# Performance work log

Measured on AMD Instinct MI355X. Metric: run time of the kernel, lower is better.

Reference implementation:

```python
import jax, jax.numpy as jnp
import numpy as np

N, D = 50000, 1000
FH1, FH2 = 256, 128
GH1, GH2, H = 64, 30, 3
NC = 10
E = 800000
BN_EPS = 1e-5


def setup_inputs() -> dict:
    key = jax.random.key(0)
    ks = iter(jax.random.split(key, 48))
    nk = lambda: next(ks)
    r = lambda *s: jax.random.normal(nk(), s, jnp.float32) * 0.05
    g = lambda n: 1.0 + jax.random.normal(nk(), (n,), jnp.float32) * 0.01
    return dict(
        x=jax.random.normal(nk(), (N, D), jnp.float32),
        edge_index=jax.random.randint(nk(), (2, E), 0, N, dtype=jnp.int32),
        enc_w1=r(D, FH1), enc_b1=r(FH1), enc_g1=g(FH1), enc_bt1=r(FH1),
        enc_w2=r(FH1, FH2), enc_b2=r(FH2), enc_g2=g(FH2), enc_bt2=r(FH2),
        gat1_w=r(FH2, H * GH1), gat1_asrc=r(H, GH1), gat1_adst=r(H, GH1), gat1_b=r(H * GH1),
        gat2_w=r(H * GH1, GH2), gat2_asrc=r(1, GH2), gat2_adst=r(1, GH2), gat2_b=r(GH2),
        gat3_w=r(H * GH1, GH2), gat3_asrc=r(1, GH2), gat3_adst=r(1, GH2), gat3_b=r(GH2),
        dec_w1=r(GH2, FH2), dec_b1=r(FH2), dec_g1=g(FH2), dec_bt1=r(FH2),
        dec_w2=r(FH2, FH1), dec_b2=r(FH1), dec_g2=g(FH1), dec_bt2=r(FH1),
        dec_w3=r(FH1, D), dec_b3=r(D),
        clu_w1=r(GH2, FH2), clu_b1=r(FH2), clu_g1=g(FH2), clu_bt1=r(FH2),
        clu_w2=r(FH2, NC), clu_b2=r(NC),
    )


def _bn_elu(h, w, b, gm, bt):
    # Linear -> BatchNorm1d (batch stats) -> ELU; dropout is identity at eval
    h = h @ w + b
    m = h.mean(0)
    v = h.var(0)
    return jax.nn.elu(gm * (h - m) * jax.lax.rsqrt(v + BN_EPS) + bt)


def _gat(h, src, dst, n, w, a_src, a_dst, b, heads, oc, concat):
    # PyG GATConv: per-head linear, edge-wise LeakyReLU(0.2) scores,
    # softmax over incoming edges of each dst node, weighted scatter-sum.
    hh = (h @ w).reshape(n, heads, oc)            # [N,H,C]
    s_src = jnp.sum(hh * a_src, -1)               # [N,H]
    s_dst = jnp.sum(hh * a_dst, -1)               # [N,H]
    e = jax.nn.leaky_relu(s_src[src] + s_dst[dst], negative_slope=0.2)  # [E,H]
    m = jax.ops.segment_max(e, dst, num_segments=n)
    p = jnp.exp(e - m[dst])
    denom = jax.ops.segment_sum(p, dst, num_segments=n)
    alpha = p / denom[dst]                        # [E,H]
    msg = hh[src] * alpha[..., None]              # [E,H,C]
    out = jax.ops.segment_sum(msg, dst, num_segments=n)
    out = out.reshape(n, heads * oc) if concat else out.mean(1)
    return out + b


def reference(x, edge_index,
              enc_w1, enc_b1, enc_g1, enc_bt1, enc_w2, enc_b2, enc_g2, enc_bt2,
              gat1_w, gat1_asrc, gat1_adst, gat1_b,
              gat2_w, gat2_asrc, gat2_adst, gat2_b,
              gat3_w, gat3_asrc, gat3_adst, gat3_b,
              dec_w1, dec_b1, dec_g1, dec_bt1, dec_w2, dec_b2, dec_g2, dec_bt2, dec_w3, dec_b3,
              clu_w1, clu_b1, clu_g1, clu_bt1, clu_w2, clu_b2):
    n = x.shape[0]
    loops = jnp.arange(n, dtype=edge_index.dtype)  # GATConv add_self_loops=True
    src = jnp.concatenate([edge_index[0], loops])
    dst = jnp.concatenate([edge_index[1], loops])

    h = _bn_elu(x, enc_w1, enc_b1, enc_g1, enc_bt1)
    h = _bn_elu(h, enc_w2, enc_b2, enc_g2, enc_bt2)
    h = jax.nn.relu(_gat(h, src, dst, n, gat1_w, gat1_asrc, gat1_adst, gat1_b, H, GH1, True))
    mu = _gat(h, src, dst, n, gat2_w, gat2_asrc, gat2_adst, gat2_b, 1, GH2, False)
    logvar = _gat(h, src, dst, n, gat3_w, gat3_asrc, gat3_adst, gat3_b, 1, GH2, False)
    z = mu  # eval-mode reparameterize returns mu

    d = _bn_elu(z, dec_w1, dec_b1, dec_g1, dec_bt1)
    d = _bn_elu(d, dec_w2, dec_b2, dec_g2, dec_bt2)
    x_rec = d @ dec_w3 + dec_b3

    c = _bn_elu(z, clu_w1, clu_b1, clu_g1, clu_bt1)
    pred = jax.nn.softmax(c @ clu_w2 + clu_b2, axis=1)
    return (pred, x_rec, z, mu, logvar)
```

## Files before the change

### kernel.cpp

```cpp
#include <hip/hip_runtime.h>
#include <hip/hip_bf16.h>

typedef short short8 __attribute__((ext_vector_type(8)));
typedef short short4v __attribute__((ext_vector_type(4)));
typedef float f32x4 __attribute__((ext_vector_type(4)));

static __device__ __forceinline__ short f2bf(float f){
  __hip_bfloat16 h = __float2bfloat16(f);
  return __builtin_bit_cast(short, h);
}
static __device__ __forceinline__ float b2f(short s){
  unsigned int u = ((unsigned int)(unsigned short)s) << 16;
  return __builtin_bit_cast(float, u);
}
static __device__ __forceinline__ float lrelu(float x){ return x > 0.f ? x : 0.2f*x; }
static __device__ __forceinline__ float eluf(float x){ return x > 0.f ? x : (__expf(x)-1.f); }
static __device__ __forceinline__ int imin(int a,int b){ return a<b?a:b; }

typedef const __attribute__((address_space(1))) void as1_void;
typedef __attribute__((address_space(3))) void as3_void;
static __device__ __forceinline__ void gload16(const void* g, void* l){
  __builtin_amdgcn_global_load_lds((as1_void*)g, (as3_void*)l, 16, 0, 0);
}
template<int NN> __device__ __forceinline__ void wait_vm(){
  if constexpr (NN==0) asm volatile("s_waitcnt vmcnt(0)" ::: "memory");
  else if constexpr (NN==3) asm volatile("s_waitcnt vmcnt(3)" ::: "memory");
  else if constexpr (NN==4) asm volatile("s_waitcnt vmcnt(4)" ::: "memory");
  else if constexpr (NN==6) asm volatile("s_waitcnt vmcnt(6)" ::: "memory");
  else if constexpr (NN==8) asm volatile("s_waitcnt vmcnt(8)" ::: "memory");
  else if constexpr (NN==12) asm volatile("s_waitcnt vmcnt(12)" ::: "memory");
  else asm volatile("s_waitcnt vmcnt(0)" ::: "memory");
}

__global__ __launch_bounds__(256) void cvt_x(const float* __restrict__ x, short* __restrict__ xb, int M){
  int row = blockIdx.x*2 + (threadIdx.x>>7);
  int c8  = (threadIdx.x&127)*8;
  if (row >= M || c8 >= 1000) return;
  const float* p = x + (size_t)row*1000 + c8;
  float4 f0 = *(const float4*)p, f1 = *(const float4*)(p+4);
  short8 o;
  o[0]=f2bf(f0.x);o[1]=f2bf(f0.y);o[2]=f2bf(f0.z);o[3]=f2bf(f0.w);
  o[4]=f2bf(f1.x);o[5]=f2bf(f1.y);o[6]=f2bf(f1.z);o[7]=f2bf(f1.w);
  *(short8*)&xb[(size_t)row*1000 + c8] = o;
}

template<int BN, bool OBF16, bool CST, bool SMAX, bool G23S>
__global__ __launch_bounds__(256) void gemm_g(
    const short* __restrict__ A, int lda, const short* __restrict__ Bt, int ldb,
    void* __restrict__ Cv, int ldc, const float* __restrict__ bias,
    int M, int N, int K, int nbn,
    float* __restrict__ o_sum, float* __restrict__ o_sq,
    float* __restrict__ s2s, float* __restrict__ s2d,
    float* __restrict__ s3s, float* __restrict__ s3d,
    const float* __restrict__ a2s, const float* __restrict__ a2d,
    const float* __restrict__ a3s, const float* __restrict__ a3d)
{
  constexpr int BM = 128, BK = 32, GPR = 4;
  constexpr int WM = BM/2, WN = BN/2;
  constexpr int FM = WM/16, FN = WN/16;
  constexpr int AI = (BM*GPR)/(4*64);
  constexpr int BI_T = (BN*GPR)/64;
  constexpr bool BDUP = (BI_T < 4);
  constexpr int BI = BDUP ? BI_T : BI_T/4;
  constexpr int LPT = AI + BI;
  constexpr int TS = (BM+BN)*BK;
  __shared__ short lds[4][TS];

  const int tid = threadIdx.x, wid = tid>>6, lane = tid&63;
  const int wm = wid>>1, wn = wid&1;
  int nwg = gridDim.x;
  int q8 = nwg >> 3, r8 = nwg & 7;
  int xcd = blockIdx.x & 7, pos = blockIdx.x >> 3;
  int wg = (xcd < r8 ? xcd*(q8+1) : r8*(q8+1) + (xcd-r8)*q8) + pos;
  int bmt = wg / nbn, bnt = wg - bmt*nbn;
  const int bm = bmt*BM, bn = bnt*BN;
  const int lr = lane&15, lg = lane>>4;
  const int nt = (K + BK - 1)/BK;

  f32x4 acc[FM][FN] = {};

  auto STAGE = [&](int t){
    int buf = t & 3, k0 = t*BK;
    #pragma unroll
    for (int i=0;i<AI;i++){
      int ci = wid*AI + i;
      int c = ci*64 + lane;
      int row = c>>2, g = c&3;
      int gr = imin(bm+row, M-1);
      const short* src = A + (size_t)gr*lda + k0 + ((g ^ (row&3))<<3);
      gload16(src, &lds[buf][ci*512]);
    }
    #pragma unroll
    for (int i=0;i<BI;i++){
      int bi = BDUP ? i : wid*BI + i;
      int c = bi*64 + lane;
      int row = c>>2, g = c&3;
      const short* src = Bt + (size_t)(bn+row)*ldb + k0 + ((g ^ (row&3))<<3);
      gload16(src, &lds[buf][BM*BK + bi*512]);
    }
  };

  for (int s=0; s<3 && s<nt; ++s) STAGE(s);

  for (int t=0; t<nt; ++t){
    int newer = imin(nt, t+3) - t - 1;
    if (newer >= 2) wait_vm<2*LPT>();
    else if (newer == 1) wait_vm<LPT>();
    else wait_vm<0>();
    __builtin_amdgcn_s_barrier();
    __builtin_amdgcn_sched_barrier(0);
    if (t+3 < nt) STAGE(t+3);
    int buf = t & 3;
    short8 af[FM], bf[FN];
    #pragma unroll
    for (int m=0;m<FM;m++){
      int r = wm*WM + m*16 + lr;
      af[m] = *(short8*)&lds[buf][r*BK + ((lg ^ (r&3))<<3)];
    }
    #pragma unroll
    for (int n=0;n<FN;n++){
      int r = wn*WN + n*16 + lr;
      bf[n] = *(short8*)&lds[buf][BM*BK + r*BK + ((lg ^ (r&3))<<3)];
    }
    #pragma unroll
    for (int m=0;m<FM;m++)
      #pragma unroll
      for (int n=0;n<FN;n++)
        acc[m][n] = __builtin_amdgcn_mfma_f32_16x16x32_bf16(af[m], bf[n], acc[m][n], 0, 0, 0);
  }

  if (SMAX){
    #pragma unroll
    for (int m=0;m<FM;m++)
      #pragma unroll
      for (int q=0;q<4;q++){
        int row = bm + wm*WM + m*16 + lg*4 + q;
        float v = (lr < 10) ? (acc[m][0][q] + bias[lr]) : -3e38f;
        float mx = v;
        #pragma unroll
        for (int d=1; d<16; d<<=1) mx = fmaxf(mx, __shfl_xor(mx, d));
        float e = (lr < 10) ? __expf(v - mx) : 0.f;
        float sm = e;
        #pragma unroll
        for (int d=1; d<16; d<<=1) sm += __shfl_xor(sm, d);
        if (wn == 0 && lr < 10 && row < M)
          ((float*)Cv)[(size_t)row*10 + lr] = e/sm;
      }
    return;
  }

  #pragma unroll
  for (int m=0;m<FM;m++)
    #pragma unroll
    for (int n=0;n<FN;n++)
      #pragma unroll
      for (int q=0;q<4;q++){
        int row = bm + wm*WM + m*16 + lg*4 + q;
        int col = bn + wn*WN + n*16 + lr;
        if (row < M && col < N){
          float v = acc[m][n][q];
          if (bias) v += bias[col];
          if (OBF16) ((short*)Cv)[(size_t)row*ldc + col] = f2bf(v);
          else       ((float*)Cv)[(size_t)row*ldc + col] = v;
        }
      }

  if (G23S){
    float a_s[FN], a_d[FN];
    #pragma unroll
    for (int n=0;n<FN;n++){
      int cl = n*16 + lr;
      bool valid = cl < 30;
      a_s[n] = valid ? (wn ? a3s[cl] : a2s[cl]) : 0.f;
      a_d[n] = valid ? (wn ? a3d[cl] : a2d[cl]) : 0.f;
    }
    #pragma unroll
    for (int m=0;m<FM;m++)
      #pragma unroll
      for (int q=0;q<4;q++){
        int row = bm + wm*WM + m*16 + lg*4 + q;
        float ps = 0.f, pd = 0.f;
        #pragma unroll
        for (int n=0;n<FN;n++){ ps += acc[m][n][q]*a_s[n]; pd += acc[m][n][q]*a_d[n]; }
        #pragma unroll
        for (int d=1; d<16; d<<=1){ ps += __shfl_xor(ps, d); pd += __shfl_xor(pd, d); }
        if (lr == 0 && row < M){
          if (wn){ s3s[row] = ps; s3d[row] = pd; }
          else   { s2s[row] = ps; s2d[row] = pd; }
        }
      }
  }

  if (CST){
    #pragma unroll
    for (int n=0;n<FN;n++){
      float s = 0.f, q2 = 0.f;
      #pragma unroll
      for (int m=0;m<FM;m++)
        #pragma unroll
        for (int q=0;q<4;q++){
          int row = bm + wm*WM + m*16 + lg*4 + q;
          if (row < M){ float v = acc[m][n][q]; s += v; q2 += v*v; }
        }
      s  += __shfl_xor(s, 16);  s += __shfl_xor(s, 32);
      q2 += __shfl_xor(q2, 16); q2 += __shfl_xor(q2, 32);
      if (lg == 0){
        int col = bn + wn*WN + n*16 + lr;
        if (col < N){ atomicAdd(&o_sum[col], s); atomicAdd(&o_sq[col], q2); }
      }
    }
  }
}

struct WEnt { const float* src; short* dst; int K, N, KP, NR; };
struct WTab { WEnt e[10]; };
__global__ __launch_bounds__(256) void wtrans_all(WTab tab){
  WEnt w = tab.e[blockIdx.y];
  int gid = blockIdx.x*256 + threadIdx.x;
  if (gid >= w.NR * w.KP) return;
  int n = gid / w.KP, k = gid - n*w.KP;
  float v = (k < w.K && n < w.N) ? w.src[(size_t)k*w.N + n] : 0.f;
  w.dst[gid] = f2bf(v);
}

template<int C>
__global__ __launch_bounds__(256) void bn_elu_apply2(const float* __restrict__ H, short* __restrict__ O,
    int M, float invM,
    const float* __restrict__ ssum, const float* __restrict__ ssq,
    const float* __restrict__ g, const float* __restrict__ bt){
  __shared__ float sc[C], sh[C];
  for (int c = threadIdx.x; c < C; c += 256){
    float mn  = ssum[c]*invM;
    float var = ssq[c]*invM - mn*mn;
    float s = g[c]*rsqrtf(var + 1e-5f);
    sc[c] = s; sh[c] = bt[c] - mn*s;
  }
  __syncthreads();
  int total4 = M*(C/4);
  for (int i = blockIdx.x*256+threadIdx.x; i < total4; i += gridDim.x*256){
    float4 v = ((const float4*)H)[i];
    int cb = (i*4) & (C-1);
    short4v o;
    o[0] = f2bf(eluf(v.x*sc[cb+0]+sh[cb+0]));
    o[1] = f2bf(eluf(v.y*sc[cb+1]+sh[cb+1]));
    o[2] = f2bf(eluf(v.z*sc[cb+2]+sh[cb+2]));
    o[3] = f2bf(eluf(v.w*sc[cb+3]+sh[cb+3]));
    ((short4v*)O)[i] = o;
  }
}

__global__ __launch_bounds__(256) void bn_elu_split(const float* __restrict__ H,
    short* __restrict__ Od, short* __restrict__ Oc, int M, float invM,
    const float* __restrict__ ssum, const float* __restrict__ ssq,
    const float* __restrict__ gd, const float* __restrict__ btd,
    const float* __restrict__ gc, const float* __restrict__ btc){
  __shared__ float sc[256], sh[256];
  {
    int c = threadIdx.x;
    float mn  = ssum[c]*invM;
    float var = ssq[c]*invM - mn*mn;
    float gg = (c<128) ? gd[c] : gc[c-128];
    float bb = (c<128) ? btd[c] : btc[c-128];
    float s = gg*rsqrtf(var + 1e-5f);
    sc[c] = s; sh[c] = bb - mn*s;
  }
  __syncthreads();
  int total4 = M*64;
  for (int i = blockIdx.x*256+threadIdx.x; i < total4; i += gridDim.x*256){
    float4 v = ((const float4*)H)[i];
    int cb = (i*4) & 255;
    short4v o;
    o[0] = f2bf(eluf(v.x*sc[cb+0]+sh[cb+0]));
    o[1] = f2bf(eluf(v.y*sc[cb+1]+sh[cb+1]));
    o[2] = f2bf(eluf(v.z*sc[cb+2]+sh[cb+2]));
    o[3] = f2bf(eluf(v.w*sc[cb+3]+sh[cb+3]));
    int row = i>>6;
    short* O = (cb < 128) ? Od : Oc;
    *(short4v*)&O[(size_t)row*128 + (cb&127)] = o;
  }
}

__global__ void hist_kernel(const int* __restrict__ d, int E, int* __restrict__ deg){
  int i = blockIdx.x*256 + threadIdx.x;
  if (i < E) atomicAdd(&deg[d[i]], 1);
}
__global__ __launch_bounds__(256) void scan1(const int* __restrict__ deg, int* __restrict__ offs,
                                             int* __restrict__ bsum, int n){
  __shared__ int sm[256];
  int tid = threadIdx.x;
  int base = blockIdx.x*1024 + tid*4;
  int v0 = base+0<n ? deg[base+0] : 0;
  int v1 = base+1<n ? deg[base+1] : 0;
  int v2 = base+2<n ? deg[base+2] : 0;
  int v3 = base+3<n ? deg[base+3] : 0;
  int ts = v0+v1+v2+v3;
  sm[tid] = ts;
  __syncthreads();
  #pragma unroll
  for (int d=1; d<256; d<<=1){
    int t = (tid>=d) ? sm[tid-d] : 0;
    __syncthreads();
    sm[tid] += t;
    __syncthreads();
  }
  int ex = sm[tid] - ts;
  if (base+0<n) offs[base+0] = ex;
  if (base+1<n) offs[base+1] = ex+v0;
  if (base+2<n) offs[base+2] = ex+v0+v1;
  if (base+3<n) offs[base+3] = ex+v0+v1+v2;
  if (tid==255) bsum[blockIdx.x] = sm[255];
}
__global__ __launch_bounds__(256) void scan3(int* __restrict__ offs, const int* __restrict__ bsum,
                      int* __restrict__ cursor, int n, int total){
  __shared__ int base_sm;
  int tgt = blockIdx.x >> 2;
  if (threadIdx.x < 64){
    int j = threadIdx.x;
    int v = (j < tgt) ? bsum[j] : 0;
    #pragma unroll
    for (int d=32; d; d>>=1) v += __shfl_xor(v, d);
    if (j == 0) base_sm = v;
  }
  __syncthreads();
  int i = blockIdx.x*256 + threadIdx.x;
  if (i < n){ int v = offs[i] + base_sm; offs[i]=v; cursor[i]=v; }
  if (i == 0) offs[n] = total;
}
__global__ void scatter_kernel(const int* __restrict__ s, const int* __restrict__ d, int E,
                               int* __restrict__ cursor, int* __restrict__ csr){
  int i = blockIdx.x*256 + threadIdx.x;
  if (i < E){ int pos = atomicAdd(&cursor[d[i]], 1); csr[pos] = s[i]; }
}

__global__ __launch_bounds__(256) void gat1_scores_bf(const short* __restrict__ hh,
    const float* __restrict__ as, const float* __restrict__ ad,
    float* __restrict__ ss, float* __restrict__ sd, int n){
  int w = threadIdx.x >> 6, lane = threadIdx.x & 63;
  int row = blockIdx.x*4 + w;
  if (row >= n) return;
  const short* hr = hh + (size_t)row*192;
  float ps[3], pd[3];
  #pragma unroll
  for (int h=0; h<3; h++){
    float v = b2f(hr[h*64 + lane]);
    ps[h] = v * as[h*64+lane];
    pd[h] = v * ad[h*64+lane];
  }
  #pragma unroll
  for (int m=32; m; m>>=1){
    #pragma unroll
    for (int h=0;h<3;h++){ ps[h] += __shfl_xor(ps[h], m); pd[h] += __shfl_xor(pd[h], m); }
  }
  if (lane == 0){
    #pragma unroll
    for (int h=0;h<3;h++){ ss[row*3+h]=ps[h]; sd[row*3+h]=pd[h]; }
  }
}

__global__ __launch_bounds__(256) void gat1_gather_bf(const int* __restrict__ offs, const int* __restrict__ csr,
    const short* __restrict__ hh, const float* __restrict__ ss, const float* __restrict__ sd,
    const float* __restrict__ bias, short* __restrict__ out, int n){
  int w = threadIdx.x >> 6, lane = threadIdx.x & 63;
  int dst = blockIdx.x*4 + w;
  if (dst >= n) return;
  float sd0 = sd[dst*3+0], sd1 = sd[dst*3+1], sd2 = sd[dst*3+2];
  float p0 = __expf(lrelu(ss[dst*3+0]+sd0));
  float p1 = __expf(lrelu(ss[dst*3+1]+sd1));
  float p2 = __expf(lrelu(ss[dst*3+2]+sd2));
  const short* hr = hh + (size_t)dst*192;
  float a0 = p0*b2f(hr[lane]), a1 = p1*b2f(hr[64+lane]), a2 = p2*b2f(hr[128+lane]);
  float d0 = p0, d1 = p1, d2 = p2;
  int p = offs[dst], pe = offs[dst+1];
  int n0=0,n1=0,n2=0,n3=0;
  if (p+4 <= pe){ n0=csr[p]; n1=csr[p+1]; n2=csr[p+2]; n3=csr[p+3]; }
  while (p+4 <= pe){
    int s0=n0, s1=n1, s2=n2, s3=n3;
    int pn = p+4;
    if (pn+4 <= pe){ n0=csr[pn]; n1=csr[pn+1]; n2=csr[pn+2]; n3=csr[pn+3]; }
    float e00=ss[s0*3+0], e01=ss[s0*3+1], e02=ss[s0*3+2];
    float e10=ss[s1*3+0], e11=ss[s1*3+1], e12=ss[s1*3+2];
    float e20=ss[s2*3+0], e21=ss[s2*3+1], e22=ss[s2*3+2];
    float e30=ss[s3*3+0], e31=ss[s3*3+1], e32=ss[s3*3+2];
    const short* r0 = hh + (size_t)s0*192;
    const short* r1 = hh + (size_t)s1*192;
    const short* r2 = hh + (size_t)s2*192;
    const short* r3 = hh + (size_t)s3*192;
    float v00=b2f(r0[lane]), v01=b2f(r0[64+lane]), v02=b2f(r0[128+lane]);
    float v10=b2f(r1[lane]), v11=b2f(r1[64+lane]), v12=b2f(r1[128+lane]);
    float v20=b2f(r2[lane]), v21=b2f(r2[64+lane]), v22=b2f(r2[128+lane]);
    float v30=b2f(r3[lane]), v31=b2f(r3[64+lane]), v32=b2f(r3[128+lane]);
    float q00=__expf(lrelu(e00+sd0)), q01=__expf(lrelu(e01+sd1)), q02=__expf(lrelu(e02+sd2));
    float q10=__expf(lrelu(e10+sd0)), q11=__expf(lrelu(e11+sd1)), q12=__expf(lrelu(e12+sd2));
    float q20=__expf(lrelu(e20+sd0)), q21=__expf(lrelu(e21+sd1)), q22=__expf(lrelu(e22+sd2));
    float q30=__expf(lrelu(e30+sd0)), q31=__expf(lrelu(e31+sd1)), q32=__expf(lrelu(e32+sd2));
    a0 += q00*v00 + q10*v10 + q20*v20 + q30*v30;
    a1 += q01*v01 + q11*v11 + q21*v21 + q31*v31;
    a2 += q02*v02 + q12*v12 + q22*v22 + q32*v32;
    d0 += q00+q10+q20+q30;
    d1 += q01+q11+q21+q31;
    d2 += q02+q12+q22+q32;
    p = pn;
  }
  for (; p < pe; ++p){
    int src = csr[p];
    float q0 = __expf(lrelu(ss[src*3+0]+sd0));
    float q1 = __expf(lrelu(ss[src*3+1]+sd1));
    float q2 = __expf(lrelu(ss[src*3+2]+sd2));
    const short* sr = hh + (size_t)src*192;
    a0 += q0*b2f(sr[lane]); a1 += q1*b2f(sr[64+lane]); a2 += q2*b2f(sr[128+lane]);
    d0 += q0; d1 += q1; d2 += q2;
  }
  float v0 = a0/d0 + bias[lane];
  float v1 = a1/d1 + bias[64+lane];
  float v2 = a2/d2 + bias[128+lane];
  short* orow = out + (size_t)dst*192;
  orow[lane]      = f2bf(v0 > 0.f ? v0 : 0.f);
  orow[64+lane]   = f2bf(v1 > 0.f ? v1 : 0.f);
  orow[128+lane]  = f2bf(v2 > 0.f ? v2 : 0.f);
}

__global__ __launch_bounds__(256) void gat23_gather(const int* __restrict__ offs, const int* __restrict__ csr,
    const float* __restrict__ hh23,
    const float* __restrict__ s2s, const float* __restrict__ s2d,
    const float* __restrict__ s3s, const float* __restrict__ s3d,
    const float* __restrict__ b2, const float* __restrict__ b3,
    float* __restrict__ zs, float* __restrict__ mus, float* __restrict__ lvs,
    short* __restrict__ zbf, int n){
  int w = threadIdx.x >> 6, lane = threadIdx.x & 63;
  int dst = blockIdx.x*4 + w;
  if (dst >= n) return;
  bool lo = lane < 32;
  int c = lane & 31;
  bool valid = c < 30;
  float sdA = s2d[dst], sdB = s3d[dst];
  float sdx = lo ? sdA : sdB;
  const float* ssx = lo ? s2s : s3s;
  float p2 = __expf(lrelu(s2s[dst]+sdA));
  float p3 = __expf(lrelu(s3s[dst]+sdB));
  float val = valid ? hh23[(size_t)dst*64+lane] : 0.f;
  float acc = (lo ? p2 : p3) * val;
  float den2 = p2, den3 = p3;
  int p = offs[dst], pe = offs[dst+1];
  int n0=0,n1=0,n2=0,n3=0;
  if (p+4 <= pe){ n0=csr[p]; n1=csr[p+1]; n2=csr[p+2]; n3=csr[p+3]; }
  while (p+4 <= pe){
    int s0=n0, s1=n1, s2i=n2, s3i=n3;
    int pn = p+4;
    if (pn+4 <= pe){ n0=csr[pn]; n1=csr[pn+1]; n2=csr[pn+2]; n3=csr[pn+3]; }
    float eA0=ssx[s0], eA1=ssx[s1], eA2=ssx[s2i], eA3=ssx[s3i];
    float f20=s2s[s0], f21=s2s[s1], f22=s2s[s2i], f23=s2s[s3i];
    float f30=s3s[s0], f31=s3s[s1], f32=s3s[s2i], f33=s3s[s3i];
    float v0 = valid ? hh23[(size_t)s0*64+lane] : 0.f;
    float v1 = valid ? hh23[(size_t)s1*64+lane] : 0.f;
    float v2 = valid ? hh23[(size_t)s2i*64+lane] : 0.f;
    float v3 = valid ? hh23[(size_t)s3i*64+lane] : 0.f;
    float qx0=__expf(lrelu(eA0+sdx)), qx1=__expf(lrelu(eA1+sdx));
    float qx2=__expf(lrelu(eA2+sdx)), qx3=__expf(lrelu(eA3+sdx));
    acc += qx0*v0 + qx1*v1 + qx2*v2 + qx3*v3;
    den2 += __expf(lrelu(f20+sdA)) + __expf(lrelu(f21+sdA)) + __expf(lrelu(f22+sdA)) + __expf(lrelu(f23+sdA));
    den3 += __expf(lrelu(f30+sdB)) + __expf(lrelu(f31+sdB)) + __expf(lrelu(f32+sdB)) + __expf(lrelu(f33+sdB));
    p = pn;
  }
  for (; p < pe; ++p){
    int src = csr[p];
    float q2 = __expf(lrelu(s2s[src]+sdA));
    float q3 = __expf(lrelu(s3s[src]+sdB));
    float v = valid ? hh23[(size_t)src*64+lane] : 0.f;
    acc += (lo ? q2 : q3) * v;
    den2 += q2; den3 += q3;
  }
  if (lo){
    if (valid){
      float v = acc/den2 + b2[c];
      zs[(size_t)dst*30+c]  = v;
      mus[(size_t)dst*30+c] = v;
      zbf[(size_t)dst*32+c] = f2bf(v);
    } else {
      zbf[(size_t)dst*32+c] = 0;
    }
  } else if (valid){
    lvs[(size_t)dst*30+c] = acc/den3 + b3[c];
  }
}

static inline int cdiv(int a, int b){ return (a + b - 1) / b; }

extern "C" void kernel_launch(void* const* d_in, const int* in_sizes, int n_in,
                              void* d_out, int out_size, void* d_ws, size_t ws_size,
                              hipStream_t stream)
{
  const float* x        = (const float*)d_in[0];
  const int*   ei       = (const int*)  d_in[1];
  const float* enc_w1   = (const float*)d_in[2];
  const float* enc_g1   = (const float*)d_in[4];
  const float* enc_bt1  = (const float*)d_in[5];
  const float* enc_w2   = (const float*)d_in[6];
  const float* enc_g2   = (const float*)d_in[8];
  const float* enc_bt2  = (const float*)d_in[9];
  const float* gat1_w   = (const float*)d_in[10];
  const float* gat1_as  = (const float*)d_in[11];
  const float* gat1_ad  = (const float*)d_in[12];
  const float* gat1_b   = (const float*)d_in[13];
  const float* gat2_w   = (const float*)d_in[14];
  const float* gat2_as  = (const float*)d_in[15];
  const float* gat2_ad  = (const float*)d_in[16];
  const float* gat2_b   = (const float*)d_in[17];
  const float* gat3_w   = (const float*)d_in[18];
  const float* gat3_as  = (const float*)d_in[19];
  const float* gat3_ad  = (const float*)d_in[20];
  const float* gat3_b   = (const float*)d_in[21];
  const float* dec_w1   = (const float*)d_in[22];
  const float* dec_g1   = (const float*)d_in[24];
  const float* dec_bt1  = (const float*)d_in[25];
  const float* dec_w2   = (const float*)d_in[26];
  const float* dec_g2   = (const float*)d_in[28];
  const float* dec_bt2  = (const float*)d_in[29];
  const float* dec_w3   = (const float*)d_in[30];
  const float* dec_b3   = (const float*)d_in[31];
  const float* clu_w1   = (const float*)d_in[32];
  const float* clu_g1   = (const float*)d_in[34];
  const float* clu_bt1  = (const float*)d_in[35];
  const float* clu_w2   = (const float*)d_in[36];
  const float* clu_b2   = (const float*)d_in[37];

  const int N = in_sizes[0] / 1000;
  const int E = in_sizes[1] / 2;
  const int* e_src = ei;
  const int* e_dst = ei + E;
  const float invN = 1.f/(float)N;

  float* out  = (float*)d_out;
  float* pred = out;
  float* xrec = out + (size_t)N*10;
  float* zs   = xrec + (size_t)N*1000;
  float* mus  = zs  + (size_t)N*30;
  float* lvs  = mus + (size_t)N*30;

  char* ws = (char*)d_ws;
  size_t off = 0;
  auto alloc = [&](size_t bytes)->char*{
    char* p = ws + off;
    off = (off + bytes + 255) & ~(size_t)255;
    return p;
  };
  short* t_enc1  = (short*)alloc(256*1024*2);
  short* t_enc2  = (short*)alloc(128*256*2);
  short* t_gat1  = (short*)alloc(256*128*2);
  short* t_gat23 = (short*)alloc(64*192*2);
  short* t_dc1   = (short*)alloc(256*32*2);
  short* t_dec2  = (short*)alloc(256*128*2);
  short* t_dec3  = (short*)alloc(1024*256*2);
  short* t_clu2  = (short*)alloc(32*128*2);
  float* h1f  = (float*)alloc((size_t)N*256*4);
  short* h1b  = (short*)alloc((size_t)N*256*2);
  float* h2f  = (float*)alloc((size_t)N*128*4);
  short* h2b  = (short*)alloc((size_t)N*128*2);
  short* hh1b = (short*)alloc((size_t)N*192*2);
  short* h3b  = (short*)alloc((size_t)N*192*2);
  float* hh23f= (float*)alloc((size_t)N*64*4);
  short* zbf  = (short*)alloc((size_t)N*32*2);
  float* ss1  = (float*)alloc((size_t)N*3*4);
  float* sd1  = (float*)alloc((size_t)N*3*4);
  float* s2s  = (float*)alloc((size_t)N*4);
  float* s2d  = (float*)alloc((size_t)N*4);
  float* s3s  = (float*)alloc((size_t)N*4);
  float* s3d  = (float*)alloc((size_t)N*4);
  float* stats= (float*)alloc(2048*4);
  int*   deg  = (int*)alloc((size_t)(N+1)*4);
  int*   offs = (int*)alloc((size_t)(N+1)*4);
  int*   curp = (int*)alloc((size_t)(N+1)*4);
  int*   bsum = (int*)alloc(256*4);
  int*   csr  = (int*)alloc((size_t)E*4);
  short* xb   = h1b;
  float* dc1f = h2f;
  short* d1b  = h3b;
  short* c1b  = (short*)hh23f;
  float* d2f  = h1f;
  short* d2b  = h1b;
  float* st_enc1 = stats, *st_enc2 = stats+512, *st_dc1 = stats+768, *st_dec2 = stats+1280;

  WTab tab;
  tab.e[0]  = {enc_w1, t_enc1, 1000, 256, 1024, 256};
  tab.e[1]  = {enc_w2, t_enc2, 256, 128, 256, 128};
  tab.e[2]  = {gat1_w, t_gat1, 128, 192, 128, 256};
  tab.e[3]  = {gat2_w, t_gat23, 192, 30, 192, 32};
  tab.e[4]  = {gat3_w, t_gat23 + 32*192, 192, 30, 192, 32};
  tab.e[5]  = {dec_w1, t_dc1, 30, 128, 32, 128};
  tab.e[6]  = {clu_w1, t_dc1 + 128*32, 30, 128, 32, 128};
  tab.e[7]  = {dec_w2, t_dec2, 128, 256, 128, 256};
  tab.e[8]  = {dec_w3, t_dec3, 256, 1000, 256, 1024};
  tab.e[9]  = {clu_w2, t_clu2, 128, 10, 128, 32};
  wtrans_all<<<dim3(1024, 10), 256, 0, stream>>>(tab);
  hipMemsetAsync(stats, 0, 2048*4, stream);
  hipMemsetAsync(deg, 0, (size_t)(N+1)*4, stream);

  hist_kernel<<<cdiv(E,256), 256, 0, stream>>>(e_dst, E, deg);
  int nb = cdiv(N, 1024);
  scan1<<<nb, 256, 0, stream>>>(deg, offs, bsum, N);
  scan3<<<cdiv(N,256), 256, 0, stream>>>(offs, bsum, curp, N, E);
  scatter_kernel<<<cdiv(E,256), 256, 0, stream>>>(e_src, e_dst, E, curp, csr);

  const int MB = cdiv(N, 128);

  cvt_x<<<cdiv(N,2), 256, 0, stream>>>(x, xb, N);
  gemm_g<128,false,true,false,false><<<MB*2, 256, 0, stream>>>(
      xb, 1000, t_enc1, 1024, h1f, 256, nullptr, N, 256, 1000, 2,
      st_enc1, st_enc1+256, nullptr,nullptr,nullptr,nullptr, nullptr,nullptr,nullptr,nullptr);
  bn_elu_apply2<256><<<2048, 256, 0, stream>>>(h1f, h1b, N, invN, st_enc1, st_enc1+256, enc_g1, enc_bt1);

  gemm_g<128,false,true,false,false><<<MB, 256, 0, stream>>>(
      h1b, 256, t_enc2, 256, h2f, 128, nullptr, N, 128, 256, 1,
      st_enc2, st_enc2+128, nullptr,nullptr,nullptr,nullptr, nullptr,nullptr,nullptr,nullptr);
  bn_elu_apply2<128><<<2048, 256, 0, stream>>>(h2f, h2b, N, invN, st_enc2, st_enc2+128, enc_g2, enc_bt2);

  gemm_g<64,true,false,false,false><<<MB*3, 256, 0, stream>>>(
      h2b, 128, t_gat1, 128, hh1b, 192, nullptr, N, 192, 128, 3,
      nullptr,nullptr, nullptr,nullptr,nullptr,nullptr, nullptr,nullptr,nullptr,nullptr);
  gat1_scores_bf<<<cdiv(N,4), 256, 0, stream>>>(hh1b, gat1_as, gat1_ad, ss1, sd1, N);
  gat1_gather_bf<<<cdiv(N,4), 256, 0, stream>>>(offs, csr, hh1b, ss1, sd1, gat1_b, h3b, N);

  gemm_g<64,false,false,false,true><<<MB, 256, 0, stream>>>(
      h3b, 192, t_gat23, 192, hh23f, 64, nullptr, N, 64, 192, 1,
      nullptr,nullptr, s2s,s2d,s3s,s3d, gat2_as,gat2_ad,gat3_as,gat3_ad);
  gat23_gather<<<cdiv(N,4), 256, 0, stream>>>(offs, csr, hh23f, s2s, s2d, s3s, s3d, gat2_b, gat3_b, zs, mus, lvs, zbf, N);

  gemm_g<128,false,true,false,false><<<MB*2, 256, 0, stream>>>(
      zbf, 32, t_dc1, 32, dc1f, 256, nullptr, N, 256, 32, 2,
      st_dc1, st_dc1+256, nullptr,nullptr,nullptr,nullptr, nullptr,nullptr,nullptr,nullptr);
  bn_elu_split<<<2048, 256, 0, stream>>>(dc1f, d1b, c1b, N, invN, st_dc1, st_dc1+256, dec_g1, dec_bt1, clu_g1, clu_bt1);

  gemm_g<128,false,true,false,false><<<MB*2, 256, 0, stream>>>(
      d1b, 128, t_dec2, 128, d2f, 256, nullptr, N, 256, 128, 2,
      st_dec2, st_dec2+256, nullptr,nullptr,nullptr,nullptr, nullptr,nullptr,nullptr,nullptr);
  bn_elu_apply2<256><<<2048, 256, 0, stream>>>(d2f, d2b, N, invN, st_dec2, st_dec2+256, dec_g2, dec_bt2);

  gemm_g<128,false,false,false,false><<<MB*8, 256, 0, stream>>>(
      d2b, 256, t_dec3, 256, xrec, 1000, dec_b3, N, 1000, 256, 8,
      nullptr,nullptr, nullptr,nullptr,nullptr,nullptr, nullptr,nullptr,nullptr,nullptr);

  gemm_g<32,false,false,true,false><<<MB, 256, 0, stream>>>(
      c1b, 128, t_clu2, 128, pred, 10, clu_b2, N, 10, 128, 1,
      nullptr,nullptr, nullptr,nullptr,nullptr,nullptr, nullptr,nullptr,nullptr,nullptr);
}
```

Baseline: 636.6 us.

## Store pre-BN GEMM outputs in bf16 and fuse GAT1 scores into GEMM epilogue

The intermediate pre-BatchNorm activations and the GAT2/3 projected features are now written as bf16 instead of fp32, which halves the bytes written by the GEMMs and read by the BN/ELU apply kernels and the gat23 gather. The separate gat1_scores kernel is removed. Its per-head attention dot products are computed in the GAT1 GEMM epilogue with shuffle reductions and atomicAdd into a score buffer, which is zeroed by an enlarged memset. The cost is lower precision in the intermediates, and the BN statistics are still taken from the fp32 accumulators.

```diff
diff --git a/kernel.cpp b/kernel.cpp
--- a/kernel.cpp
+++ b/kernel.cpp
@@ -28,7 +28,6 @@
   else if constexpr (NN==4) asm volatile("s_waitcnt vmcnt(4)" ::: "memory");
   else if constexpr (NN==6) asm volatile("s_waitcnt vmcnt(6)" ::: "memory");
   else if constexpr (NN==8) asm volatile("s_waitcnt vmcnt(8)" ::: "memory");
-  else if constexpr (NN==12) asm volatile("s_waitcnt vmcnt(12)" ::: "memory");
   else asm volatile("s_waitcnt vmcnt(0)" ::: "memory");
 }
 
@@ -44,7 +43,7 @@
   *(short8*)&xb[(size_t)row*1000 + c8] = o;
 }
 
-template<int BN, bool OBF16, bool CST, bool SMAX, bool G23S>
+template<int BN, bool OBF16, bool CST, bool SMAX, bool G23S, bool G1S>
 __global__ __launch_bounds__(256) void gemm_g(
     const short* __restrict__ A, int lda, const short* __restrict__ Bt, int ldb,
     void* __restrict__ Cv, int ldc, const float* __restrict__ bias,
@@ -165,6 +164,32 @@
         }
       }
 
+  if (G1S){
+    int h = bnt;
+    float a_s[FN], a_d[FN];
+    #pragma unroll
+    for (int n=0;n<FN;n++){
+      int cl = wn*WN + n*16 + lr;
+      a_s[n] = a2s[h*64 + cl];
+      a_d[n] = a2d[h*64 + cl];
+    }
+    #pragma unroll
+    for (int m=0;m<FM;m++)
+      #pragma unroll
+      for (int q=0;q<4;q++){
+        int row = bm + wm*WM + m*16 + lg*4 + q;
+        float ps = 0.f, pd = 0.f;
+        #pragma unroll
+        for (int n=0;n<FN;n++){ ps += acc[m][n][q]*a_s[n]; pd += acc[m][n][q]*a_d[n]; }
+        #pragma unroll
+        for (int d=1; d<16; d<<=1){ ps += __shfl_xor(ps, d); pd += __shfl_xor(pd, d); }
+        if (lr == 0 && row < M){
+          atomicAdd(&s2s[row*3+h], ps);
+          atomicAdd(&s2d[row*3+h], pd);
+        }
+      }
+  }
+
   if (G23S){
     float a_s[FN], a_d[FN];
     #pragma unroll
@@ -224,7 +249,7 @@
 }
 
 template<int C>
-__global__ __launch_bounds__(256) void bn_elu_apply2(const float* __restrict__ H, short* __restrict__ O,
+__global__ __launch_bounds__(256) void bn_elu_apply2(const short* __restrict__ H, short* __restrict__ O,
     int M, float invM,
     const float* __restrict__ ssum, const float* __restrict__ ssq,
     const float* __restrict__ g, const float* __restrict__ bt){
@@ -236,20 +261,18 @@
     sc[c] = s; sh[c] = bt[c] - mn*s;
   }
   __syncthreads();
-  int total4 = M*(C/4);
-  for (int i = blockIdx.x*256+threadIdx.x; i < total4; i += gridDim.x*256){
-    float4 v = ((const float4*)H)[i];
-    int cb = (i*4) & (C-1);
-    short4v o;
-    o[0] = f2bf(eluf(v.x*sc[cb+0]+sh[cb+0]));
-    o[1] = f2bf(eluf(v.y*sc[cb+1]+sh[cb+1]));
-    o[2] = f2bf(eluf(v.z*sc[cb+2]+sh[cb+2]));
-    o[3] = f2bf(eluf(v.w*sc[cb+3]+sh[cb+3]));
-    ((short4v*)O)[i] = o;
-  }
-}
-
-__global__ __launch_bounds__(256) void bn_elu_split(const float* __restrict__ H,
+  int total8 = M*(C/8);
+  for (int i = blockIdx.x*256+threadIdx.x; i < total8; i += gridDim.x*256){
+    short8 v = ((const short8*)H)[i];
+    int cb = (i*8) & (C-1);
+    short8 o;
+    #pragma unroll
+    for (int j=0;j<8;j++) o[j] = f2bf(eluf(b2f(v[j])*sc[cb+j]+sh[cb+j]));
+    ((short8*)O)[i] = o;
+  }
+}
+
+__global__ __launch_bounds__(256) void bn_elu_split(const short* __restrict__ H,
     short* __restrict__ Od, short* __restrict__ Oc, int M, float invM,
     const float* __restrict__ ssum, const float* __restrict__ ssq,
     const float* __restrict__ gd, const float* __restrict__ btd,
@@ -265,18 +288,16 @@
     sc[c] = s; sh[c] = bb - mn*s;
   }
   __syncthreads();
-  int total4 = M*64;
-  for (int i = blockIdx.x*256+threadIdx.x; i < total4; i += gridDim.x*256){
-    float4 v = ((const float4*)H)[i];
-    int cb = (i*4) & 255;
-    short4v o;
-    o[0] = f2bf(eluf(v.x*sc[cb+0]+sh[cb+0]));
-    o[1] = f2bf(eluf(v.y*sc[cb+1]+sh[cb+1]));
-    o[2] = f2bf(eluf(v.z*sc[cb+2]+sh[cb+2]));
-    o[3] = f2bf(eluf(v.w*sc[cb+3]+sh[cb+3]));
-    int row = i>>6;
+  int total8 = M*32;
+  for (int i = blockIdx.x*256+threadIdx.x; i < total8; i += gridDim.x*256){
+    short8 v = ((const short8*)H)[i];
+    int cb = (i*8) & 255;
+    short8 o;
+    #pragma unroll
+    for (int j=0;j<8;j++) o[j] = f2bf(eluf(b2f(v[j])*sc[cb+j]+sh[cb+j]));
+    int row = i>>5;
     short* O = (cb < 128) ? Od : Oc;
-    *(short4v*)&O[(size_t)row*128 + (cb&127)] = o;
+    *(short8*)&O[(size_t)row*128 + (cb&127)] = o;
   }
 }
 
@@ -330,31 +351,6 @@
                                int* __restrict__ cursor, int* __restrict__ csr){
   int i = blockIdx.x*256 + threadIdx.x;
   if (i < E){ int pos = atomicAdd(&cursor[d[i]], 1); csr[pos] = s[i]; }
-}
-
-__global__ __launch_bounds__(256) void gat1_scores_bf(const short* __restrict__ hh,
-    const float* __restrict__ as, const float* __restrict__ ad,
-    float* __restrict__ ss, float* __restrict__ sd, int n){
-  int w = threadIdx.x >> 6, lane = threadIdx.x & 63;
-  int row = blockIdx.x*4 + w;
-  if (row >= n) return;
-  const short* hr = hh + (size_t)row*192;
-  float ps[3], pd[3];
-  #pragma unroll
-  for (int h=0; h<3; h++){
-    float v = b2f(hr[h*64 + lane]);
-    ps[h] = v * as[h*64+lane];
-    pd[h] = v * ad[h*64+lane];
-  }
-  #pragma unroll
-  for (int m=32; m; m>>=1){
-    #pragma unroll
-    for (int h=0;h<3;h++){ ps[h] += __shfl_xor(ps[h], m); pd[h] += __shfl_xor(pd[h], m); }
-  }
-  if (lane == 0){
-    #pragma unroll
-    for (int h=0;h<3;h++){ ss[row*3+h]=ps[h]; sd[row*3+h]=pd[h]; }
-  }
 }
 
 __global__ __launch_bounds__(256) void gat1_gather_bf(const int* __restrict__ offs, const int* __restrict__ csr,
@@ -420,7 +416,7 @@
 }
 
 __global__ __launch_bounds__(256) void gat23_gather(const int* __restrict__ offs, const int* __restrict__ csr,
-    const float* __restrict__ hh23,
+    const short* __restrict__ hh23,
     const float* __restrict__ s2s, const float* __restrict__ s2d,
     const float* __restrict__ s3s, const float* __restrict__ s3d,
     const float* __restrict__ b2, const float* __restrict__ b3,
@@ -437,7 +433,7 @@
   const float* ssx = lo ? s2s : s3s;
   float p2 = __expf(lrelu(s2s[dst]+sdA));
   float p3 = __expf(lrelu(s3s[dst]+sdB));
-  float val = valid ? hh23[(size_t)dst*64+lane] : 0.f;
+  float val = valid ? b2f(hh23[(size_t)dst*64+lane]) : 0.f;
   float acc = (lo ? p2 : p3) * val;
   float den2 = p2, den3 = p3;
   int p = offs[dst], pe = offs[dst+1];
@@ -450,10 +446,10 @@
     float eA0=ssx[s0], eA1=ssx[s1], eA2=ssx[s2i], eA3=ssx[s3i];
     float f20=s2s[s0], f21=s2s[s1], f22=s2s[s2i], f23=s2s[s3i];
     float f30=s3s[s0], f31=s3s[s1], f32=s3s[s2i], f33=s3s[s3i];
-    float v0 = valid ? hh23[(size_t)s0*64+lane] : 0.f;
-    float v1 = valid ? hh23[(size_t)s1*64+lane] : 0.f;
-    float v2 = valid ? hh23[(size_t)s2i*64+lane] : 0.f;
-    float v3 = valid ? hh23[(size_t)s3i*64+lane] : 0.f;
+    float v0 = valid ? b2f(hh23[(size_t)s0*64+lane]) : 0.f;
+    float v1 = valid ? b2f(hh23[(size_t)s1*64+lane]) : 0.f;
+    float v2 = valid ? b2f(hh23[(size_t)s2i*64+lane]) : 0.f;
+    float v3 = valid ? b2f(hh23[(size_t)s3i*64+lane]) : 0.f;
     float qx0=__expf(lrelu(eA0+sdx)), qx1=__expf(lrelu(eA1+sdx));
     float qx2=__expf(lrelu(eA2+sdx)), qx3=__expf(lrelu(eA3+sdx));
     acc += qx0*v0 + qx1*v1 + qx2*v2 + qx3*v3;
@@ -465,7 +461,7 @@
     int src = csr[p];
     float q2 = __expf(lrelu(s2s[src]+sdA));
     float q3 = __expf(lrelu(s3s[src]+sdB));
-    float v = valid ? hh23[(size_t)src*64+lane] : 0.f;
+    float v = valid ? b2f(hh23[(size_t)src*64+lane]) : 0.f;
     acc += (lo ? q2 : q3) * v;
     den2 += q2; den3 += q3;
   }
@@ -559,24 +555,27 @@
   short* h3b  = (short*)alloc((size_t)N*192*2);
   float* hh23f= (float*)alloc((size_t)N*64*4);
   short* zbf  = (short*)alloc((size_t)N*32*2);
-  float* ss1  = (float*)alloc((size_t)N*3*4);
-  float* sd1  = (float*)alloc((size_t)N*3*4);
+  float* stats= (float*)alloc((2048 + (size_t)6*N)*4);
+  float* ss1  = stats + 2048;
+  float* sd1  = ss1 + (size_t)3*N;
   float* s2s  = (float*)alloc((size_t)N*4);
   float* s2d  = (float*)alloc((size_t)N*4);
   float* s3s  = (float*)alloc((size_t)N*4);
   float* s3d  = (float*)alloc((size_t)N*4);
-  float* stats= (float*)alloc(2048*4);
   int*   deg  = (int*)alloc((size_t)(N+1)*4);
   int*   offs = (int*)alloc((size_t)(N+1)*4);
   int*   curp = (int*)alloc((size_t)(N+1)*4);
   int*   bsum = (int*)alloc(256*4);
   int*   csr  = (int*)alloc((size_t)E*4);
-  short* xb   = h1b;
-  float* dc1f = h2f;
-  short* d1b  = h3b;
-  short* c1b  = (short*)hh23f;
-  float* d2f  = h1f;
-  short* d2b  = h1b;
+  short* xb     = h1b;
+  short* h1pre  = (short*)h1f;
+  short* h2pre  = (short*)h2f;
+  short* hh23b  = (short*)hh23f;
+  short* dc1pre = (short*)h2f;
+  short* d1b    = h3b;
+  short* c1b    = hh1b;
+  short* d2pre  = (short*)h1f;
+  short* d2b    = h1b;
   float* st_enc1 = stats, *st_enc2 = stats+512, *st_dc1 = stats+768, *st_dec2 = stats+1280;
 
   WTab tab;
@@ -591,7 +590,7 @@
   tab.e[8]  = {dec_w3, t_dec3, 256, 1000, 256, 1024};
   tab.e[9]  = {clu_w2, t_clu2, 128, 10, 128, 32};
   wtrans_all<<<dim3(1024, 10), 256, 0, stream>>>(tab);
-  hipMemsetAsync(stats, 0, 2048*4, stream);
+  hipMemsetAsync(stats, 0, (2048 + (size_t)6*N)*4, stream);
   hipMemsetAsync(deg, 0, (size_t)(N+1)*4, stream);
 
   hist_kernel<<<cdiv(E,256), 256, 0, stream>>>(e_dst, E, deg);
@@ -603,42 +602,41 @@
   const int MB = cdiv(N, 128);
 
   cvt_x<<<cdiv(N,2), 256, 0, stream>>>(x, xb, N);
-  gemm_g<128,false,true,false,false><<<MB*2, 256, 0, stream>>>(
-      xb, 1000, t_enc1, 1024, h1f, 256, nullptr, N, 256, 1000, 2,
+  gemm_g<128,true,true,false,false,false><<<MB*2, 256, 0, stream>>>(
+      xb, 1000, t_enc1, 1024, h1pre, 256, nullptr, N, 256, 1000, 2,
       st_enc1, st_enc1+256, nullptr,nullptr,nullptr,nullptr, nullptr,nullptr,nullptr,nullptr);
-  bn_elu_apply2<256><<<2048, 256, 0, stream>>>(h1f, h1b, N, invN, st_enc1, st_enc1+256, enc_g1, enc_bt1);
-
-  gemm_g<128,false,true,false,false><<<MB, 256, 0, stream>>>(
-      h1b, 256, t_enc2, 256, h2f, 128, nullptr, N, 128, 256, 1,
+  bn_elu_apply2<256><<<2048, 256, 0, stream>>>(h1pre, h1b, N, invN, st_enc1, st_enc1+256, enc_g1, enc_bt1);
+
+  gemm_g<128,true,true,false,false,false><<<MB, 256, 0, stream>>>(
+      h1b, 256, t_enc2, 256, h2pre, 128, nullptr, N, 128, 256, 1,
       st_enc2, st_enc2+128, nullptr,nullptr,nullptr,nullptr, nullptr,nullptr,nullptr,nullptr);
-  bn_elu_apply2<128><<<2048, 256, 0, stream>>>(h2f, h2b, N, invN, st_enc2, st_enc2+128, enc_g2, enc_bt2);
-
-  gemm_g<64,true,false,false,false><<<MB*3, 256, 0, stream>>>(
+  bn_elu_apply2<128><<<2048, 256, 0, stream>>>(h2pre, h2b, N, invN, st_enc2, st_enc2+128, enc_g2, enc_bt2);
+
+  gemm_g<64,true,false,false,false,true><<<MB*3, 256, 0, stream>>>(
       h2b, 128, t_gat1, 128, hh1b, 192, nullptr, N, 192, 128, 3,
-      nullptr,nullptr, nullptr,nullptr,nullptr,nullptr, nullptr,nullptr,nullptr,nullptr);
-  gat1_scores_bf<<<cdiv(N,4), 256, 0, stream>>>(hh1b, gat1_as, gat1_ad, ss1, sd1, N);
+      nullptr,nullptr, ss1,sd1,nullptr,nullptr, gat1_as,gat1_ad,nullptr,nullptr);
   gat1_gather_bf<<<cdiv(N,4), 256, 0, stream>>>(offs, csr, hh1b, ss1, sd1, gat1_b, h3b, N);
 
-  gemm_g<64,false,false,false,true><<<MB, 256, 0, stream>>>(
-      h3b, 192, t_gat23, 192, hh23f, 64, nullptr, N, 64, 192, 1,
+  gemm_g<64,true,false,false,true,false><<<MB, 256, 0, stream>>>(
+      h3b, 192, t_gat23, 192, hh23b, 64, nullptr, N, 64, 192, 1,
       nullptr,nullptr, s2s,s2d,s3s,s3d, gat2_as,gat2_ad,gat3_as,gat3_ad);
-  gat23_gather<<<cdiv(N,4), 256, 0, stream>>>(offs, csr, hh23f, s2s, s2d, s3s, s3d, gat2_b, gat3_b, zs, mus, lvs, zbf, N);
-
-  gemm_g<128,false,true,false,false><<<MB*2, 256, 0, stream>>>(
-      zbf, 32, t_dc1, 32, dc1f, 256, nullptr, N, 256, 32, 2,
+  gat23_gather<<<cdiv(N,4), 256, 0, stream>>>(offs, csr, hh23b, s2s, s2d, s3s, s3d, gat2_b, gat3_b, zs, mus, lvs, zbf, N);
+
+  gemm_g<128,true,true,false,false,false><<<MB*2, 256, 0, stream>>>(
+      zbf, 32, t_dc1, 32, dc1pre, 256, nullptr, N, 256, 32, 2,
       st_dc1, st_dc1+256, nullptr,nullptr,nullptr,nullptr, nullptr,nullptr,nullptr,nullptr);
-  bn_elu_split<<<2048, 256, 0, stream>>>(dc1f, d1b, c1b, N, invN, st_dc1, st_dc1+256, dec_g1, dec_bt1, clu_g1, clu_bt1);
-
-  gemm_g<128,false,true,false,false><<<MB*2, 256, 0, stream>>>(
-      d1b, 128, t_dec2, 128, d2f, 256, nullptr, N, 256, 128, 2,
+  bn_elu_split<<<2048, 256, 0, stream>>>(dc1pre, d1b, c1b, N, invN, st_dc1, st_dc1+256, dec_g1, dec_bt1, clu_g1, clu_bt1);
+
+  gemm_g<128,true,true,false,false,false><<<MB*2, 256, 0, stream>>>(
+      d1b, 128, t_dec2, 128, d2pre, 256, nullptr, N, 256, 128, 2,
       st_dec2, st_dec2+256, nullptr,nullptr,nullptr,nullptr, nullptr,nullptr,nullptr,nullptr);
-  bn_elu_apply2<256><<<2048, 256, 0, stream>>>(d2f, d2b, N, invN, st_dec2, st_dec2+256, dec_g2, dec_bt2);
-
-  gemm_g<128,false,false,false,false><<<MB*8, 256, 0, stream>>>(
+  bn_elu_apply2<256><<<2048, 256, 0, stream>>>(d2pre, d2b, N, invN, st_dec2, st_dec2+256, dec_g2, dec_bt2);
+
+  gemm_g<128,false,false,false,false,false><<<MB*8, 256, 0, stream>>>(
       d2b, 256, t_dec3, 256, xrec, 1000, dec_b3, N, 1000, 256, 8,
       nullptr,nullptr, nullptr,nullptr,nullptr,nullptr, nullptr,nullptr,nullptr,nullptr);
 
-  gemm_g<32,false,false,true,false><<<MB, 256, 0, stream>>>(
+  gemm_g<32,false,false,true,false,false><<<MB, 256, 0, stream>>>(
       c1b, 128, t_clu2, 128, pred, 10, clu_b2, N, 10, 128, 1,
       nullptr,nullptr, nullptr,nullptr,nullptr,nullptr, nullptr,nullptr,nullptr,nullptr);
 }
```

After: 632.7 us. About the same (-0.6%).
